# Optimization experiments

Measured on AMD Instinct MI355X. Metric: run time of the kernel, lower is better.

Reference implementation:

```python
import jax, jax.numpy as jnp
import numpy as np

ALPHA = 0.2  # LeakyReLU negative slope


def setup_inputs() -> dict:
    key = jax.random.key(0)
    k1, k2, k3 = jax.random.split(key, 3)
    B, N, D_in, D_out = 16, 2048, 128, 128
    x = jax.random.normal(k1, (B, N, D_in), dtype=jnp.float32)
    # xavier-uniform-ish scale for params
    W = jax.random.normal(k2, (D_in, D_out), dtype=jnp.float32) * (1.414 / np.sqrt(D_in + D_out))
    a = jax.random.normal(k3, (2 * D_out, 1), dtype=jnp.float32) * (1.414 / np.sqrt(2 * D_out + 1))
    return {"x": x, "W": W, "a": a}


def reference(x, W, a):
    # h: (B, N, D)
    h = jnp.matmul(x, W)
    D = h.shape[-1]
    # a = [a1; a2]; e[b,i,j] = leakyrelu(a1 . h_i + a2 . h_j)
    a1 = a[:D, 0]   # (D,)
    a2 = a[D:, 0]   # (D,)
    s1 = jnp.einsum('bnd,d->bn', h, a1)  # (B, N) source term
    s2 = jnp.einsum('bnd,d->bn', h, a2)  # (B, N) target term
    e = jax.nn.leaky_relu(s1[:, :, None] + s2[:, None, :], negative_slope=ALPHA)  # (B, N, N)
    attention = jax.nn.softmax(e, axis=2)
    h_prime = jnp.matmul(attention, h)  # (B, N, D)
    return jax.nn.relu(h_prime)  # concat=True -> relu
```

## Files before the change

### kernel.cpp

```cpp
#include <hip/hip_runtime.h>
#include <hip/hip_bf16.h>
#include <cstddef>

#define GAT_B 16
#define GAT_N 2048
#define GAT_D 128
#define GAT_ROWS (GAT_B * GAT_N)
#define CH 256
#define CL 8
#define GAT_ALPHA 0.2f

typedef __attribute__((ext_vector_type(8))) short short8v;
typedef __attribute__((ext_vector_type(4))) float f32x4;

__device__ __forceinline__ void cvt_hilo(float x, unsigned short& hi, unsigned short& lo) {
  union { float f; unsigned u; } a;
  a.f = x;
  hi = (unsigned short)(a.u >> 16);
  union { unsigned u; float f; } b;
  b.u = (unsigned)hi << 16;
  union { float f; unsigned u; } c;
  c.f = x - b.f;
  lo = (unsigned short)(c.u >> 16);
}

__global__ __launch_bounds__(256) void k0_wfrag(const float* __restrict__ W,
                                                unsigned short* __restrict__ WfH,
                                                unsigned short* __restrict__ WfL) {
  const int t = blockIdx.x * 256 + threadIdx.x;
  const int n = t & 127, g = (t >> 7) & 3, ks = t >> 9;
  short8v vh, vl;
#pragma unroll
  for (int j = 0; j < 8; ++j) {
    const int k = ks * 32 + g * 8 + j;
    unsigned short hi, lo;
    cvt_hilo(W[k * 128 + n], hi, lo);
    vh[j] = (short)hi;
    vl[j] = (short)lo;
  }
  *(short8v*)&WfH[t * 8] = vh;
  *(short8v*)&WfL[t * 8] = vl;
}

__global__ __launch_bounds__(256) void k1_gemm(const float* __restrict__ x,
                                               const unsigned short* __restrict__ WfHg,
                                               const unsigned short* __restrict__ WfLg,
                                               const float* __restrict__ aa,
                                               float* __restrict__ h,
                                               float* __restrict__ s1part,
                                               float* __restrict__ s2part) {
  __shared__ unsigned short xH[64 * 128];
  __shared__ unsigned short xL[64 * 128];
  const int tid = threadIdx.x;
  const int row0 = blockIdx.x * 64;

#pragma unroll
  for (int p = 0; p < 8; ++p) {
    const int row = p * 8 + (tid >> 5);
    const int f4 = tid & 31;
    const float4 v = ((const float4*)(x + (size_t)(row0 + row) * GAT_D))[f4];
    unsigned short h0, h1, h2, h3, l0, l1, l2, l3;
    cvt_hilo(v.x, h0, l0);
    cvt_hilo(v.y, h1, l1);
    cvt_hilo(v.z, h2, l2);
    cvt_hilo(v.w, h3, l3);
    const int slot = (f4 >> 1) ^ (row & 7);
    const int base = row * 128 + slot * 8 + (f4 & 1) * 4;
    *(ushort4*)&xH[base] = make_ushort4(h0, h1, h2, h3);
    *(ushort4*)&xL[base] = make_ushort4(l0, l1, l2, l3);
  }

  const int w = tid >> 6, l = tid & 63;
  const int wc0 = w * 32;
  const int g = l >> 4, c16 = l & 15;

  short8v bh[4][2], bl[4][2];
#pragma unroll
  for (int ks = 0; ks < 4; ++ks)
#pragma unroll
    for (int nt = 0; nt < 2; ++nt) {
      const int bi = ((ks * 4 + g) * 128 + wc0 + nt * 16 + c16) * 8;
      bh[ks][nt] = *(const short8v*)&WfHg[bi];
      bl[ks][nt] = *(const short8v*)&WfLg[bi];
    }

  __syncthreads();

  f32x4 acc[4][2];
#pragma unroll
  for (int mt = 0; mt < 4; ++mt)
#pragma unroll
    for (int nt = 0; nt < 2; ++nt) acc[mt][nt] = (f32x4)(0.f);

#pragma unroll
  for (int ks = 0; ks < 4; ++ks) {
    short8v ah[4], al[4];
#pragma unroll
    for (int mt = 0; mt < 4; ++mt) {
      const int row = mt * 16 + c16;
      const int ai = row * 128 + (((ks * 4 + g) ^ (row & 7)) * 8);
      ah[mt] = *(const short8v*)&xH[ai];
      al[mt] = *(const short8v*)&xL[ai];
    }
#pragma unroll
    for (int mt = 0; mt < 4; ++mt) {
#pragma unroll
      for (int nt = 0; nt < 2; ++nt) {
        acc[mt][nt] = __builtin_amdgcn_mfma_f32_16x16x32_bf16(ah[mt], bh[ks][nt], acc[mt][nt], 0, 0, 0);
        acc[mt][nt] = __builtin_amdgcn_mfma_f32_16x16x32_bf16(al[mt], bh[ks][nt], acc[mt][nt], 0, 0, 0);
        acc[mt][nt] = __builtin_amdgcn_mfma_f32_16x16x32_bf16(ah[mt], bl[ks][nt], acc[mt][nt], 0, 0, 0);
      }
    }
  }

#pragma unroll
  for (int mt = 0; mt < 4; ++mt)
#pragma unroll
    for (int nt = 0; nt < 2; ++nt)
#pragma unroll
      for (int j = 0; j < 4; ++j)
        h[(size_t)(row0 + mt * 16 + g * 4 + j) * GAT_D + wc0 + nt * 16 + c16] =
            acc[mt][nt][j];

  float a1v[2], a2v[2];
#pragma unroll
  for (int nt = 0; nt < 2; ++nt) {
    a1v[nt] = aa[wc0 + nt * 16 + c16];
    a2v[nt] = aa[128 + wc0 + nt * 16 + c16];
  }
#pragma unroll
  for (int mt = 0; mt < 4; ++mt) {
#pragma unroll
    for (int j = 0; j < 4; ++j) {
      float t1 = acc[mt][0][j] * a1v[0] + acc[mt][1][j] * a1v[1];
      float t2 = acc[mt][0][j] * a2v[0] + acc[mt][1][j] * a2v[1];
#pragma unroll
      for (int off = 1; off < 16; off <<= 1) {
        t1 += __shfl_xor(t1, off);
        t2 += __shfl_xor(t2, off);
      }
      if (c16 == 0) {
        const int row = row0 + mt * 16 + g * 4 + j;
        s1part[w * GAT_ROWS + row] = t1;
        s2part[w * GAT_ROWS + row] = t2;
      }
    }
  }
}

__global__ __launch_bounds__(1024) void k2_sort(const float* __restrict__ s1part,
                                                const float* __restrict__ s2part,
                                                float* __restrict__ s2s,
                                                int* __restrict__ idxs,
                                                float* __restrict__ s1s,
                                                int* __restrict__ rids,
                                                float* __restrict__ wA,
                                                float* __restrict__ wP,
                                                float* __restrict__ preDenA,
                                                float* __restrict__ sufDenP) {
  __shared__ float v[2048];
  __shared__ int id[2048];
  __shared__ float wtotA[16];
  __shared__ float wtotP[16];
  const int tid = threadIdx.x;
  const int b = blockIdx.x >> 1;
  const int half = blockIdx.x & 1;
  const int i0 = tid, i1 = tid + 1024;
  const float* src = (half == 0) ? s2part : s1part;
  {
    const int r0 = b * GAT_N + i0, r1 = b * GAT_N + i1;
    float v0 = src[r0] + src[GAT_ROWS + r0] + src[2 * GAT_ROWS + r0] + src[3 * GAT_ROWS + r0];
    float v1 = src[r1] + src[GAT_ROWS + r1] + src[2 * GAT_ROWS + r1] + src[3 * GAT_ROWS + r1];
    if (half == 1) {
      v0 = -v0;
      v1 = -v1;
    }
    v[i0] = v0;
    v[i1] = v1;
  }
  __syncthreads();

  const int lane = tid & 63;
  const int e0 = ((tid >> 6) << 7) + lane * 2;
  const int e1 = e0 + 1;
  float va = v[e0], vb = v[e1];
  int ida = e0, idb = e1;

  auto lanex = [&](int k, int j) {
    const int jl = j >> 1;
    const bool dir = (e0 & k) == 0;
    const bool lower = (lane & jl) == 0;
    const bool keepMax = lower ^ dir;
    {
      const float ov = __shfl_xor(va, jl);
      const int oid = __shfl_xor(ida, jl);
      const bool ogt = (ov > va) || (ov == va && oid > ida);
      if (ogt == keepMax) { va = ov; ida = oid; }
    }
    {
      const float ov = __shfl_xor(vb, jl);
      const int oid = __shfl_xor(idb, jl);
      const bool ogt = (ov > vb) || (ov == vb && oid > idb);
      if (ogt == keepMax) { vb = ov; idb = oid; }
    }
  };
  auto pairx = [&](int k) {
    const bool dir = (e0 & k) == 0;
    const bool bgt = (vb > va) || (vb == va && idb > ida);
    if (bgt != dir) {
      const float tv = va; va = vb; vb = tv;
      const int ti = ida; ida = idb; idb = ti;
    }
  };

#pragma unroll
  for (int k = 2; k <= 128; k <<= 1) {
#pragma unroll
    for (int j = k >> 1; j >= 2; j >>= 1) lanex(k, j);
    pairx(k);
  }
  v[e0] = va; id[e0] = ida;
  v[e1] = vb; id[e1] = idb;
  __syncthreads();

  for (int k = 256; k <= 2048; k <<= 1) {
    for (int j = k >> 1; j >= 128; j >>= 1) {
      const int i = ((tid & ~(j - 1)) << 1) | (tid & (j - 1));
      const int ixj = i | j;
      const bool up = (i & k) == 0;
      const float x0 = v[i], x1 = v[ixj];
      if (up ? (x0 > x1) : (x0 < x1)) {
        v[i] = x1;
        v[ixj] = x0;
        const int ti = id[i];
        id[i] = id[ixj];
        id[ixj] = ti;
      }
      __syncthreads();
    }
    va = v[e0]; ida = id[e0];
    vb = v[e1]; idb = id[e1];
#pragma unroll
    for (int j = 64; j >= 2; j >>= 1) lanex(k, j);
    pairx(k);
    v[e0] = va; id[e0] = ida;
    v[e1] = vb; id[e1] = idb;
    __syncthreads();
  }

  if (half == 1) {
    s1s[b * GAT_N + i0] = -v[i0];
    s1s[b * GAT_N + i1] = -v[i1];
    rids[b * GAT_N + i0] = id[i0];
    rids[b * GAT_N + i1] = id[i1];
    return;
  }
  s2s[b * GAT_N + i0] = v[i0];
  s2s[b * GAT_N + i1] = v[i1];
  idxs[b * GAT_N + i0] = id[i0];
  idxs[b * GAT_N + i1] = id[i1];

  const int w = tid >> 6;
  const float aL = __expf(GAT_ALPHA * v[2 * tid]);
  const float aR = __expf(GAT_ALPHA * v[2 * tid + 1]);
  const float pL = __expf(v[2047 - 2 * tid]);
  const float pR = __expf(v[2046 - 2 * tid]);
  wA[b * GAT_N + 2 * tid] = aL;
  wA[b * GAT_N + 2 * tid + 1] = aR;
  wP[b * GAT_N + 2047 - 2 * tid] = pL;
  wP[b * GAT_N + 2046 - 2 * tid] = pR;
  float sA = aL + aR, sP = pL + pR;
#pragma unroll
  for (int off = 1; off < 64; off <<= 1) {
    const float tA = __shfl_up(sA, off);
    const float tP = __shfl_up(sP, off);
    if (lane >= off) {
      sA += tA;
      sP += tP;
    }
  }
  if (lane == 63) {
    wtotA[w] = sA;
    wtotP[w] = sP;
  }
  __syncthreads();
  float offA = 0.f, offP = 0.f;
  for (int ww = 0; ww < w; ++ww) {
    offA += wtotA[ww];
    offP += wtotP[ww];
  }
  const float inclA = offA + sA;
  const float inclP = offP + sP;
  preDenA[b * GAT_N + 2 * tid] = inclA - aR;
  preDenA[b * GAT_N + 2 * tid + 1] = inclA;
  sufDenP[b * GAT_N + 2047 - 2 * tid] = inclP - pR;
  sufDenP[b * GAT_N + 2046 - 2 * tid] = inclP;
}

__global__ __launch_bounds__(128) void k3_permute(const float* __restrict__ h,
                                                  const int* __restrict__ idxs,
                                                  const float* __restrict__ wA,
                                                  const float* __restrict__ wP,
                                                  float* __restrict__ hs,
                                                  float* __restrict__ partA,
                                                  float* __restrict__ partP) {
  const int b = blockIdx.x >> 7, cc = blockIdx.x & 127;
  const int d = threadIdx.x;
  const int* idxb = idxs + b * GAT_N;
  const float* hb = h + (size_t)b * GAT_N * GAT_D;
#pragma unroll
  for (int sub = 0; sub < 2; ++sub) {
    const int c = cc * 2 + sub;
    const int q0 = c * CL;
    float accA = 0.f, accP = 0.f;
#pragma unroll
    for (int qq = 0; qq < CL; ++qq) {
      const int q = q0 + qq;
      const int j = idxb[q];
      const float hv = hb[(size_t)j * GAT_D + d];
      hs[((size_t)b * GAT_N + q) * GAT_D + d] = hv;
      accA = fmaf(wA[b * GAT_N + q], hv, accA);
      accP = fmaf(wP[b * GAT_N + q], hv, accP);
    }
    partA[(b * CH + c) * GAT_D + d] = accA;
    partP[(b * CH + c) * GAT_D + d] = accP;
  }
}

__global__ __launch_bounds__(1024) void k3b_prep(const float* __restrict__ s1s,
                                                 const float* __restrict__ s2s,
                                                 const float* __restrict__ preDenA,
                                                 const float* __restrict__ sufDenP,
                                                 const float* __restrict__ partA,
                                                 const float* __restrict__ partP,
                                                 float* __restrict__ baseA,
                                                 float* __restrict__ baseP,
                                                 int* __restrict__ pArr,
                                                 float* __restrict__ c1,
                                                 float* __restrict__ c2) {
  __shared__ float totA[8][128];
  __shared__ float totP[8][128];
  __shared__ float sh[2048];
  const int b = blockIdx.x >> 1;
  const int role = blockIdx.x & 1;
  const int t = threadIdx.x;
  if (role == 0) {
    const int d = t & 127, g = t >> 7;
    const float* pA = partA + (size_t)(b * CH + g * 32) * GAT_D + d;
    const float* pP = partP + (size_t)(b * CH + g * 32) * GAT_D + d;
    float sA = 0.f, sP = 0.f;
#pragma unroll 8
    for (int i = 0; i < 32; ++i) {
      sA += pA[i * GAT_D];
      sP += pP[i * GAT_D];
    }
    totA[g][d] = sA;
    totP[g][d] = sP;
    __syncthreads();
    float offA = 0.f, offP = 0.f;
    for (int gg = 0; gg < g; ++gg) offA += totA[gg][d];
    for (int gg = g + 1; gg < 8; ++gg) offP += totP[gg][d];
    float run = offA;
#pragma unroll 8
    for (int i = 0; i < 32; ++i) {
      baseA[(size_t)(b * (CH + 1) + g * 32 + i) * GAT_D + d] = run;
      run += pA[i * GAT_D];
    }
    if (g == 7) baseA[(size_t)(b * (CH + 1) + CH) * GAT_D + d] = run;
    run = offP;
#pragma unroll 8
    for (int i = 31; i >= 0; --i) {
      baseP[(size_t)(b * CH + g * 32 + i) * GAT_D + d] = run;
      run += pP[i * GAT_D];
    }
  } else {
    sh[t] = s2s[b * GAT_N + t];
    sh[t + 1024] = s2s[b * GAT_N + t + 1024];
    __syncthreads();
#pragma unroll
    for (int rr = 0; rr < 2; ++rr) {
      const int j = t + rr * 1024;
      const float s1v = s1s[b * GAT_N + j];
      const float tt = -s1v;
      int lo = 0, hi = GAT_N;
      while (lo < hi) {
        const int mid = (lo + hi) >> 1;
        if (sh[mid] < tt)
          lo = mid + 1;
        else
          hi = mid;
      }
      const float e1 = __expf(s1v), e2 = __expf(GAT_ALPHA * s1v);
      float den = 0.f;
      if (lo < GAT_N) den += e1 * sufDenP[b * GAT_N + lo];
      if (lo > 0) den += e2 * preDenA[b * GAT_N + lo - 1];
      const float inv = 1.f / den;
      pArr[b * GAT_N + j] = lo;
      c1[b * GAT_N + j] = e1 * inv;
      c2[b * GAT_N + j] = e2 * inv;
    }
  }
}

__global__ __launch_bounds__(256) void k5_out(const float* __restrict__ hs,
                                              const float* __restrict__ wA,
                                              const float* __restrict__ wP,
                                              const float* __restrict__ baseA,
                                              const float* __restrict__ baseP,
                                              const int* __restrict__ pArr,
                                              const float* __restrict__ c1,
                                              const float* __restrict__ c2,
                                              const int* __restrict__ rids,
                                              float* __restrict__ out) {
  const int wave = threadIdx.x >> 6, lane = threadIdx.x & 63;
  const int j = blockIdx.x * 4 + wave;
  const int b = j >> 11;
  const int jr = b * GAT_N + (j & 2047);
  const int p = pArr[jr];
  const float cc1 = c1[jr], cc2 = c2[jr];
  const int rid = rids[jr];
  const float2* hs2 = (const float2*)(hs + (size_t)b * GAT_N * GAT_D);
  const float* wAb = wA + b * GAT_N;
  const float* wPb = wP + b * GAT_N;

  const int cA = p >> 3;
  float2 accA = ((const float2*)(baseA + (size_t)(b * (CH + 1) + cA) * GAT_D))[lane];
#pragma unroll 4
  for (int q = cA * CL; q < p; ++q) {
    const float w = wAb[q];
    const float2 hv = hs2[(size_t)q * 64 + lane];
    accA.x = fmaf(w, hv.x, accA.x);
    accA.y = fmaf(w, hv.y, accA.y);
  }

  const int pP = p < GAT_N ? p : GAT_N - 1;
  const int cP = pP >> 3;
  float2 accP = ((const float2*)(baseP + (size_t)(b * CH + cP) * GAT_D))[lane];
  const int qend = cP * CL + CL;
#pragma unroll 4
  for (int q = p; q < qend; ++q) {
    const float w = wPb[q];
    const float2 hv = hs2[(size_t)q * 64 + lane];
    accP.x = fmaf(w, hv.x, accP.x);
    accP.y = fmaf(w, hv.y, accP.y);
  }

  const float vx = cc2 * accA.x + cc1 * accP.x;
  const float vy = cc2 * accA.y + cc1 * accP.y;
  ((float2*)out)[(size_t)(b * GAT_N + rid) * 64 + lane] =
      make_float2(fmaxf(vx, 0.f), fmaxf(vy, 0.f));
}

extern "C" void kernel_launch(void* const* d_in, const int* in_sizes, int n_in,
                              void* d_out, int out_size, void* d_ws, size_t ws_size,
                              hipStream_t stream) {
  (void)in_sizes;
  (void)n_in;
  (void)out_size;
  (void)ws_size;
  const float* x = (const float*)d_in[0];
  const float* W = (const float*)d_in[1];
  const float* a = (const float*)d_in[2];
  float* out = (float*)d_out;
  float* wsf = (float*)d_ws;

  const size_t HN = (size_t)GAT_ROWS * GAT_D;
  size_t o = 0;
  float* s1part = wsf + o;   o += 4 * GAT_ROWS;
  float* s2part = wsf + o;   o += 4 * GAT_ROWS;
  float* s2s = wsf + o;      o += GAT_ROWS;
  int* idxs = (int*)(wsf + o); o += GAT_ROWS;
  float* s1s = wsf + o;      o += GAT_ROWS;
  int* rids = (int*)(wsf + o); o += GAT_ROWS;
  float* preDenA = wsf + o;  o += GAT_ROWS;
  float* sufDenP = wsf + o;  o += GAT_ROWS;
  float* wAr = wsf + o;      o += GAT_ROWS;
  float* wPr = wsf + o;      o += GAT_ROWS;
  int* pArr = (int*)(wsf + o); o += GAT_ROWS;
  float* c1 = wsf + o;       o += GAT_ROWS;
  float* c2 = wsf + o;       o += GAT_ROWS;
  float* partA = wsf + o;    o += (size_t)GAT_B * CH * GAT_D;
  float* partP = wsf + o;    o += (size_t)GAT_B * CH * GAT_D;
  float* baseA = wsf + o;    o += (size_t)GAT_B * (CH + 1) * GAT_D;
  float* baseP = wsf + o;    o += (size_t)GAT_B * CH * GAT_D;
  unsigned short* WfH = (unsigned short*)(wsf + o); o += 8192;
  unsigned short* WfL = (unsigned short*)(wsf + o); o += 8192;
  float* h = wsf + o;        o += HN;
  float* hs = wsf + o;       o += HN;

  k0_wfrag<<<8, 256, 0, stream>>>(W, WfH, WfL);
  k1_gemm<<<512, 256, 0, stream>>>(x, WfH, WfL, a, h, s1part, s2part);
  k2_sort<<<2 * GAT_B, 1024, 0, stream>>>(s1part, s2part, s2s, idxs, s1s, rids, wAr, wPr,
                                          preDenA, sufDenP);
  k3_permute<<<GAT_B * 128, 128, 0, stream>>>(h, idxs, wAr, wPr, hs, partA, partP);
  k3b_prep<<<2 * GAT_B, 1024, 0, stream>>>(s1s, s2s, preDenA, sufDenP, partA, partP,
                                           baseA, baseP, pArr, c1, c2);
  k5_out<<<GAT_ROWS / 4, 256, 0, stream>>>(hs, wAr, wPr, baseA, baseP, pArr, c1, c2,
                                           rids, out);
}
```

Baseline: 70.32 us.

## Halve prefix chunk length and vectorize permute and output kernels with float4

Changes the chunk size for the sorted prefix/suffix sums from 8 rows to 4, doubling the number of partial-sum chunks. The permute kernel now covers four chunks per block using 128-bit loads and stores. The output kernel handles its fixed 4-row chunk with two half-waves, using predicated weights and a cross-half shuffle reduction in place of variable-length loops. This cuts per-row serial gather work and divergence, but doubles the partial and base arrays that the prep kernel must scan and write.

```diff
diff --git a/kernel.cpp b/kernel.cpp
--- a/kernel.cpp
+++ b/kernel.cpp
@@ -6,8 +6,8 @@
 #define GAT_N 2048
 #define GAT_D 128
 #define GAT_ROWS (GAT_B * GAT_N)
-#define CH 256
-#define CL 8
+#define CH 512
+#define CL 4
 #define GAT_ALPHA 0.2f
 
 typedef __attribute__((ext_vector_type(8))) short short8v;
@@ -305,26 +305,29 @@
                                                   float* __restrict__ partA,
                                                   float* __restrict__ partP) {
   const int b = blockIdx.x >> 7, cc = blockIdx.x & 127;
-  const int d = threadIdx.x;
+  const int t = threadIdx.x;
+  const int cs = t >> 5, f4 = t & 31;
+  const int c = cc * 4 + cs;
+  const int q0 = c * CL;
   const int* idxb = idxs + b * GAT_N;
   const float* hb = h + (size_t)b * GAT_N * GAT_D;
-#pragma unroll
-  for (int sub = 0; sub < 2; ++sub) {
-    const int c = cc * 2 + sub;
-    const int q0 = c * CL;
-    float accA = 0.f, accP = 0.f;
-#pragma unroll
-    for (int qq = 0; qq < CL; ++qq) {
-      const int q = q0 + qq;
-      const int j = idxb[q];
-      const float hv = hb[(size_t)j * GAT_D + d];
-      hs[((size_t)b * GAT_N + q) * GAT_D + d] = hv;
-      accA = fmaf(wA[b * GAT_N + q], hv, accA);
-      accP = fmaf(wP[b * GAT_N + q], hv, accP);
-    }
-    partA[(b * CH + c) * GAT_D + d] = accA;
-    partP[(b * CH + c) * GAT_D + d] = accP;
-  }
+  f32x4 accA = (f32x4)(0.f), accP = (f32x4)(0.f);
+#pragma unroll
+  for (int qq = 0; qq < CL; ++qq) {
+    const int q = q0 + qq;
+    const int jdx = idxb[q];
+    const f32x4 hv = *(const f32x4*)(hb + (size_t)jdx * GAT_D + f4 * 4);
+    *(f32x4*)(hs + ((size_t)b * GAT_N + q) * GAT_D + f4 * 4) = hv;
+    const float wa = wA[b * GAT_N + q];
+    const float wp = wP[b * GAT_N + q];
+#pragma unroll
+    for (int e = 0; e < 4; ++e) {
+      accA[e] = fmaf(wa, hv[e], accA[e]);
+      accP[e] = fmaf(wp, hv[e], accP[e]);
+    }
+  }
+  *(f32x4*)(partA + (size_t)(b * CH + c) * GAT_D + f4 * 4) = accA;
+  *(f32x4*)(partP + (size_t)(b * CH + c) * GAT_D + f4 * 4) = accP;
 }
 
 __global__ __launch_bounds__(1024) void k3b_prep(const float* __restrict__ s1s,
@@ -346,11 +349,11 @@
   const int t = threadIdx.x;
   if (role == 0) {
     const int d = t & 127, g = t >> 7;
-    const float* pA = partA + (size_t)(b * CH + g * 32) * GAT_D + d;
-    const float* pP = partP + (size_t)(b * CH + g * 32) * GAT_D + d;
+    const float* pA = partA + (size_t)(b * CH + g * 64) * GAT_D + d;
+    const float* pP = partP + (size_t)(b * CH + g * 64) * GAT_D + d;
     float sA = 0.f, sP = 0.f;
 #pragma unroll 8
-    for (int i = 0; i < 32; ++i) {
+    for (int i = 0; i < 64; ++i) {
       sA += pA[i * GAT_D];
       sP += pP[i * GAT_D];
     }
@@ -362,15 +365,15 @@
     for (int gg = g + 1; gg < 8; ++gg) offP += totP[gg][d];
     float run = offA;
 #pragma unroll 8
-    for (int i = 0; i < 32; ++i) {
-      baseA[(size_t)(b * (CH + 1) + g * 32 + i) * GAT_D + d] = run;
+    for (int i = 0; i < 64; ++i) {
+      baseA[(size_t)(b * (CH + 1) + g * 64 + i) * GAT_D + d] = run;
       run += pA[i * GAT_D];
     }
     if (g == 7) baseA[(size_t)(b * (CH + 1) + CH) * GAT_D + d] = run;
     run = offP;
 #pragma unroll 8
-    for (int i = 31; i >= 0; --i) {
-      baseP[(size_t)(b * CH + g * 32 + i) * GAT_D + d] = run;
+    for (int i = 63; i >= 0; --i) {
+      baseP[(size_t)(b * CH + g * 64 + i) * GAT_D + d] = run;
       run += pP[i * GAT_D];
     }
   } else {
@@ -419,36 +422,42 @@
   const int p = pArr[jr];
   const float cc1 = c1[jr], cc2 = c2[jr];
   const int rid = rids[jr];
-  const float2* hs2 = (const float2*)(hs + (size_t)b * GAT_N * GAT_D);
+  const int half = lane >> 5, l32 = lane & 31;
+  int c = p >> 2;
+  if (c > CH - 1) c = CH - 1;
+  const int q0 = c * CL;
+  const float* hsb = hs + (size_t)b * GAT_N * GAT_D;
   const float* wAb = wA + b * GAT_N;
   const float* wPb = wP + b * GAT_N;
 
-  const int cA = p >> 3;
-  float2 accA = ((const float2*)(baseA + (size_t)(b * (CH + 1) + cA) * GAT_D))[lane];
-#pragma unroll 4
-  for (int q = cA * CL; q < p; ++q) {
-    const float w = wAb[q];
-    const float2 hv = hs2[(size_t)q * 64 + lane];
-    accA.x = fmaf(w, hv.x, accA.x);
-    accA.y = fmaf(w, hv.y, accA.y);
-  }
-
-  const int pP = p < GAT_N ? p : GAT_N - 1;
-  const int cP = pP >> 3;
-  float2 accP = ((const float2*)(baseP + (size_t)(b * CH + cP) * GAT_D))[lane];
-  const int qend = cP * CL + CL;
-#pragma unroll 4
-  for (int q = p; q < qend; ++q) {
-    const float w = wPb[q];
-    const float2 hv = hs2[(size_t)q * 64 + lane];
-    accP.x = fmaf(w, hv.x, accP.x);
-    accP.y = fmaf(w, hv.y, accP.y);
-  }
-
-  const float vx = cc2 * accA.x + cc1 * accP.x;
-  const float vy = cc2 * accA.y + cc1 * accP.y;
-  ((float2*)out)[(size_t)(b * GAT_N + rid) * 64 + lane] =
-      make_float2(fmaxf(vx, 0.f), fmaxf(vy, 0.f));
+  f32x4 aA = (f32x4)(0.f), aP = (f32x4)(0.f);
+#pragma unroll
+  for (int it = 0; it < 2; ++it) {
+    const int q = q0 + it * 2 + half;
+    const float wa = (q < p) ? wAb[q] : 0.f;
+    const float wp = (q >= p) ? wPb[q] : 0.f;
+    const f32x4 hv = *(const f32x4*)(hsb + (size_t)q * GAT_D + l32 * 4);
+#pragma unroll
+    for (int e = 0; e < 4; ++e) {
+      aA[e] = fmaf(wa, hv[e], aA[e]);
+      aP[e] = fmaf(wp, hv[e], aP[e]);
+    }
+  }
+#pragma unroll
+  for (int e = 0; e < 4; ++e) {
+    aA[e] += __shfl_xor(aA[e], 32);
+    aP[e] += __shfl_xor(aP[e], 32);
+  }
+
+  if (half == 0) {
+    const f32x4 bA = *(const f32x4*)(baseA + (size_t)(b * (CH + 1) + c) * GAT_D + l32 * 4);
+    const f32x4 bP = *(const f32x4*)(baseP + (size_t)(b * CH + c) * GAT_D + l32 * 4);
+    f32x4 r;
+#pragma unroll
+    for (int e = 0; e < 4; ++e)
+      r[e] = fmaxf(cc2 * (bA[e] + aA[e]) + cc1 * (bP[e] + aP[e]), 0.f);
+    *(f32x4*)(out + (size_t)(b * GAT_N + rid) * GAT_D + l32 * 4) = r;
+  }
 }
 
 extern "C" void kernel_launch(void* const* d_in, const int* in_sizes, int n_in,
```

Result: slower. 74.92 us (+6.5%).
